# Kernel optimization log

Measured on AMD Instinct MI355X. Metric: run time of the kernel, lower is better.

The kernel has to match this reference:

```python
import jax, jax.numpy as jnp
import numpy as np

B, C_IN, T, H, W = 8, 8, 12, 128, 128
HID = 32
K = 3


def _conv2d(x, w, b):
    # x: (B, Cin, H, W), w: (Cout, Cin, K, K) -> SAME padding, stride 1
    y = jax.lax.conv_general_dilated(
        x, w, window_strides=(1, 1), padding='SAME',
        dimension_numbers=('NCHW', 'OIHW', 'NCHW'))
    return y + b[None, :, None, None]


def setup_inputs() -> dict:
    key = jax.random.key(0)
    k1, k2, k3, k4, k5 = jax.random.split(key, 5)
    x = jax.random.normal(k1, (B, C_IN, T, H, W), dtype=jnp.float32)
    cin = C_IN + HID
    scale = 1.0 / np.sqrt(cin * K * K)
    W_gates = jax.random.normal(k2, (2 * HID, cin, K, K), dtype=jnp.float32) * scale
    b_gates = jax.random.normal(k3, (2 * HID,), dtype=jnp.float32) * 0.01
    W_can = jax.random.normal(k4, (HID, cin, K, K), dtype=jnp.float32) * scale
    b_can = jax.random.normal(k5, (HID,), dtype=jnp.float32) * 0.01
    return {"x": x, "W_gates": W_gates, "b_gates": b_gates,
            "W_can": W_can, "b_can": b_can}


def reference(x, W_gates, b_gates, W_can, b_can):
    # x: (B, C, T, H, W) -> swap to time-major for the recurrence
    xs = jnp.transpose(x, (2, 0, 1, 3, 4))  # (T, B, C, H, W)
    h0 = jnp.zeros((x.shape[0], HID, x.shape[3], x.shape[4]), dtype=x.dtype)

    def step(h, x_t):
        comb = jnp.concatenate([x_t, h], axis=1)          # (B, C+HID, H, W)
        gates = jax.nn.sigmoid(_conv2d(comb, W_gates, b_gates))
        reset, update = jnp.split(gates, 2, axis=1)       # each (B, HID, H, W)
        comb2 = jnp.concatenate([x_t, reset * h], axis=1)
        cand = jnp.tanh(_conv2d(comb2, W_can, b_can))
        h_next = (1.0 - update) * h + update * cand
        return h_next, h_next

    h_last, ys = jax.lax.scan(step, h0, xs)               # ys: (T, B, HID, H, W)
    out = jnp.transpose(ys, (1, 2, 0, 3, 4))              # (B, HID, T, H, W) — swap back
    return out, h_last
```

## Files before the change

kernel.cpp:

```cpp
#include <hip/hip_runtime.h>
#include <hip/hip_bf16.h>
#include <hip/hip_fp16.h>
#include <cmath>

#define BB   8
#define CIN  8
#define TT   12
#define HH   128
#define WW   128
#define HID  32
#define CCOMB 40
#define HW   (HH * WW)
#define NBLK 512

#define S1    44
#define T1W   20
#define OFF2  17600
#define S2    36
#define OFFU  29264
#define SMEM_U16 38480

typedef __attribute__((ext_vector_type(8))) short sv8;
typedef __attribute__((ext_vector_type(4))) short sv4;
typedef __attribute__((ext_vector_type(4))) float f32x4;
typedef unsigned short u16;
typedef unsigned long long ull;

__device__ inline u16 f2bf(float f) {
    union { float f; unsigned u; } v; v.f = f;
    unsigned u = v.u;
    return (u16)((u + 0x7FFFu + ((u >> 16) & 1u)) >> 16);
}
__device__ inline float bf2f(u16 h) {
    union { unsigned u; float f; } v; v.u = ((unsigned)h) << 16; return v.f;
}
__device__ inline float sigmoid_fast(float x) { return 1.f / (1.f + __expf(-x)); }
__device__ inline float tanh_fast(float z) {
    float a = fabsf(z);
    float r = 1.f - 2.f / (__expf(2.f * a) + 1.f);
    return copysignf(r, z);
}

__device__ __forceinline__ void band_rc(int i, int& r, int& c) {
    if (i < 40)      { r = i / 20;            c = i % 20; }
    else if (i < 80) { int j = i - 40; r = 18 + j / 20; c = j % 20; }
    else             { int j = i - 80; r = 2 + (j >> 2);
                       int k = j & 3;  c = (k < 2) ? k : 16 + k; }
}

__device__ inline sv8 gather_wfrag(const float* __restrict__ W,
                                   int co, int g, int kx, int ks) {
    int k0 = ks * 32 + g * 8;
    sv8 f;
    if (k0 < 120) {
        int ky  = k0 / 40;
        int ci0 = k0 - ky * 40;
#pragma unroll
        for (int i = 0; i < 8; ++i)
            f[i] = (short)f2bf(W[(((size_t)co * CCOMB + ci0 + i) * 3 + ky) * 3 + kx]);
    } else {
#pragma unroll
        for (int i = 0; i < 8; ++i) f[i] = 0;
    }
    return f;
}

__global__ void pack_weights(const float* __restrict__ Wg,
                             const float* __restrict__ Wc,
                             u16* __restrict__ pack) {
    int tid = blockIdx.x * blockDim.x + threadIdx.x;
    if (tid >= 6 * 12 * 64) return;
    int lane = tid & 63;
    int f    = (tid >> 6) % 12;
    int Gall = tid / (12 * 64);
    int kx = f >> 2, ks = f & 3;
    int g = lane >> 4;
    sv8 v;
    if (Gall < 4) v = gather_wfrag(Wg, Gall * 16 + (lane & 15), g, kx, ks);
    else          v = gather_wfrag(Wc, (Gall - 4) * 16 + (lane & 15), g, kx, ks);
    *(sv8*)&pack[(size_t)tid * 8] = v;
}

__global__ __launch_bounds__(256) void x_to_bf16(const float* __restrict__ x,
                                                 u16* __restrict__ xbf) {
    int gid = blockIdx.x * 256 + threadIdx.x;
    if (gid >= BB * TT * HW) return;
    int p  = gid & (HW - 1);
    int bt = gid >> 14;
    int t = bt % TT, b = bt / TT;
    sv8 v;
#pragma unroll
    for (int c = 0; c < 8; ++c)
        v[c] = (short)f2bf(x[(((size_t)b * CIN + c) * TT + t) * HW + p]);
    *(sv8*)&xbf[(size_t)gid * 8] = v;
}

__global__ __launch_bounds__(256, 2) void gru_persist(
    const u16* __restrict__ xbf, const u16* __restrict__ wpack,
    const float* __restrict__ bg, const float* __restrict__ bc,
    u16* __restrict__ hG, int* __restrict__ flags,
    float* __restrict__ out, float* __restrict__ hlast)
{
    __shared__ __align__(16) u16 smem[SMEM_U16];
    const int id = blockIdx.x;
    const int b = id & 7, tau = id >> 3;
    const int bx = tau & 7, by = tau >> 3;
    const int x0 = bx * 16, y0 = by * 16;
    const int tid = threadIdx.x, lane = tid & 63, w = tid >> 6;
    const int m = lane & 15, g = lane >> 4;

    int nbr = -1;
    if (tid < 8) {
        const int dxs[8] = {-1, 0, 1, -1, 1, -1, 0, 1};
        const int dys[8] = {-1, -1, -1, 0, 0, 1, 1, 1};
        int nx = bx + dxs[tid], ny = by + dys[tid];
        if ((unsigned)nx < 8u && (unsigned)ny < 8u)
            nbr = ((ny * 8 + nx) * 8 + b);
    }

    int kyv[4], ci0v[4], koff1[4], coffC[4], kstrC[4];
    bool isX[4];
#pragma unroll
    for (int ks = 0; ks < 4; ++ks) {
        int k0 = ks * 32 + g * 8;
        int ky = 0, ci0 = 0;
        if (k0 < 120) { ky = k0 / 40; ci0 = k0 - ky * 40; }
        kyv[ks] = ky; ci0v[ks] = ci0;
        koff1[ks] = ky * (T1W * S1) + ci0;
        isX[ks]   = (ci0 == 0);
        coffC[ks] = isX[ks] ? ky * (T1W * S1) : ky * (18 * S2) + (ci0 - 8);
        kstrC[ks] = isX[ks] ? S1 : S2;
    }

    const int coPair = w >> 1;
    const int parity = w & 1;
    const int co0A = coPair * 32 + g * 4;
    const int co0B = co0A + 16;
    const int grpA = coPair * 2, grpB = grpA + 1;

    for (int i = tid; i < 3200; i += 256) {
        int px = i >> 3, q = i & 7;
        *(ull*)&smem[px * S1 + 8 + q * 4] = 0ull;
    }

    const u16* xbB = xbf + (size_t)b * TT * HW * 8;
    const size_t planeElems = (size_t)BB * HW * 32;

    for (int t = 0; t < TT; ++t) {
        const u16* hGr = hG + (size_t)(t & 1) * planeElems + (size_t)b * HW * 32;
        u16*       hGw = hG + (size_t)((t + 1) & 1) * planeElems + (size_t)b * HW * 32;

        sv8 wfA[12], wfB[12];
#pragma unroll
        for (int f = 0; f < 12; ++f) {
            wfA[f] = *(const sv8*)&wpack[(((size_t)grpA * 12 + f) * 64 + lane) * 8];
            wfB[f] = *(const sv8*)&wpack[(((size_t)grpB * 12 + f) * 64 + lane) * 8];
        }

        const u16* xb = xbB + (size_t)t * HW * 8;
        for (int idx = tid; idx < 400; idx += 256) {
            int r = idx / 20, c = idx - r * 20;
            int gy = y0 + r - 2, gx = x0 + c - 2;
            sv8 v = {};
            if ((unsigned)gy < 128u && (unsigned)gx < 128u)
                v = *(const sv8*)&xb[(size_t)(gy * WW + gx) * 8];
            *(sv4*)&smem[idx * S1]     = __builtin_shufflevector(v, v, 0,1,2,3);
            *(sv4*)&smem[idx * S1 + 4] = __builtin_shufflevector(v, v, 4,5,6,7);
        }

        if (t > 0) {
            if (tid < 8 && nbr >= 0) {
                while (__hip_atomic_load(&flags[nbr * 32], __ATOMIC_RELAXED,
                                         __HIP_MEMORY_SCOPE_AGENT) < t)
                    __builtin_amdgcn_s_sleep(8);
            }
            __syncthreads();
        }

        for (int idx = tid; idx < 1152; idx += 256) {
            int i = idx >> 3, q = idx & 7;
            int r, c; band_rc(i, r, c);
            int gy = y0 + r - 2, gx = x0 + c - 2;
            ull v = 0;
            if ((unsigned)gy < 128u && (unsigned)gx < 128u)
                v = __hip_atomic_load((const ull*)&hGr[(size_t)(gy * WW + gx) * 32 + q * 4],
                                      __ATOMIC_RELAXED, __HIP_MEMORY_SCOPE_AGENT);
            *(ull*)&smem[(r * T1W + c) * S1 + 8 + q * 4] = v;
        }
        __syncthreads();

        f32x4 bgA = *(const f32x4*)&bg[co0A];
        f32x4 bgB = *(const f32x4*)&bg[co0B];
        for (int nt = parity; nt < 21; nt += 2) {
            int px = nt * 16 + m;
            bool val = px < 324;
            if (!val) px = 323;
            int yy = px / 18, xx = px - yy * 18;
            int pb = (yy * T1W + xx) * S1;
            f32x4 aA = {0.f,0.f,0.f,0.f}, aB = {0.f,0.f,0.f,0.f};
#pragma unroll
            for (int kx = 0; kx < 3; ++kx)
#pragma unroll
                for (int ks = 0; ks < 4; ++ks) {
                    int a = pb + kx * S1 + koff1[ks];
                    sv4 lo = *(const sv4*)&smem[a];
                    sv4 hi = *(const sv4*)&smem[a + 4];
                    sv8 bv = __builtin_shufflevector(lo, hi, 0,1,2,3,4,5,6,7);
                    aA = __builtin_amdgcn_mfma_f32_16x16x32_bf16(wfA[kx*4+ks], bv, aA, 0, 0, 0);
                    aB = __builtin_amdgcn_mfma_f32_16x16x32_bf16(wfB[kx*4+ks], bv, aB, 0, 0, 0);
                }
            if (coPair == 0) {
                int ctr = pb + 21 * S1 + 8;
                sv4 h4A = *(const sv4*)&smem[ctr + co0A];
                sv4 h4B = *(const sv4*)&smem[ctr + co0B];
                sv4 rhA, rhB;
#pragma unroll
                for (int r = 0; r < 4; ++r) {
                    rhA[r] = (short)f2bf(sigmoid_fast(aA[r] + bgA[r]) * bf2f((u16)h4A[r]));
                    rhB[r] = (short)f2bf(sigmoid_fast(aB[r] + bgB[r]) * bf2f((u16)h4B[r]));
                }
                if (val) {
                    *(sv4*)&smem[OFF2 + px * S2 + co0A] = rhA;
                    *(sv4*)&smem[OFF2 + px * S2 + co0B] = rhB;
                }
            } else {
                sv4 uA, uB;
#pragma unroll
                for (int r = 0; r < 4; ++r) {
                    uA[r] = (short)__half_as_ushort(__float2half(sigmoid_fast(aA[r] + bgA[r])));
                    uB[r] = (short)__half_as_ushort(__float2half(sigmoid_fast(aB[r] + bgB[r])));
                }
                if (val && yy >= 1 && yy <= 16 && xx >= 1 && xx <= 16) {
                    int ub = OFFU + ((yy - 1) * 16 + (xx - 1)) * S2;
                    *(sv4*)&smem[ub + (co0A - 32)] = uA;
                    *(sv4*)&smem[ub + (co0B - 32)] = uB;
                }
            }
        }

        sv8 wcA[12], wcB[12];
#pragma unroll
        for (int f = 0; f < 12; ++f) {
            wcA[f] = *(const sv8*)&wpack[(((size_t)4 * 12 + f) * 64 + lane) * 8];
            wcB[f] = *(const sv8*)&wpack[(((size_t)5 * 12 + f) * 64 + lane) * 8];
        }
        __syncthreads();

        const int j0 = w * 4;
        int rowb1[4], rowb2[4];
#pragma unroll
        for (int jr = 0; jr < 4; ++jr) {
            rowb1[jr] = ((j0 + jr + 1) * T1W + m + 1) * S1;
            rowb2[jr] = OFF2 + ((j0 + jr) * 18 + m) * S2;
        }
        f32x4 a2A[4], a2B[4];
#pragma unroll
        for (int jr = 0; jr < 4; ++jr) {
            a2A[jr] = (f32x4){0.f,0.f,0.f,0.f};
            a2B[jr] = (f32x4){0.f,0.f,0.f,0.f};
        }
#pragma unroll
        for (int kx = 0; kx < 3; ++kx)
#pragma unroll
            for (int ks = 0; ks < 4; ++ks) {
#pragma unroll
                for (int jr = 0; jr < 4; ++jr) {
                    int a = (isX[ks] ? rowb1[jr] : rowb2[jr]) + coffC[ks] + kx * kstrC[ks];
                    sv4 lo = *(const sv4*)&smem[a];
                    sv4 hi = *(const sv4*)&smem[a + 4];
                    sv8 bv = __builtin_shufflevector(lo, hi, 0,1,2,3,4,5,6,7);
                    a2A[jr] = __builtin_amdgcn_mfma_f32_16x16x32_bf16(wcA[kx*4+ks], bv, a2A[jr], 0, 0, 0);
                    a2B[jr] = __builtin_amdgcn_mfma_f32_16x16x32_bf16(wcB[kx*4+ks], bv, a2B[jr], 0, 0, 0);
                }
            }

        f32x4 bcA = *(const f32x4*)&bc[g * 4];
        f32x4 bcB = *(const f32x4*)&bc[16 + g * 4];
        const int cA = g * 4, cB = 16 + g * 4;
#pragma unroll
        for (int jr = 0; jr < 4; ++jr) {
            int j = j0 + jr;
            int gy = y0 + j, gx = x0 + m;
            int ctr = ((j + 2) * T1W + m + 2) * S1 + 8;
            int ub  = OFFU + (j * 16 + m) * S2;
            sv4 h4A = *(const sv4*)&smem[ctr + cA];
            sv4 h4B = *(const sv4*)&smem[ctr + cB];
            sv4 u4A = *(const sv4*)&smem[ub + cA];
            sv4 u4B = *(const sv4*)&smem[ub + cB];
            sv4 hnA, hnB;
#pragma unroll
            for (int r = 0; r < 4; ++r) {
                float cv = tanh_fast(a2A[jr][r] + bcA[r]);
                float uu = __half2float(__ushort_as_half((u16)u4A[r]));
                float hn = (1.f - uu) * bf2f((u16)h4A[r]) + uu * cv;
                a2A[jr][r] = hn; hnA[r] = (short)f2bf(hn);
                cv = tanh_fast(a2B[jr][r] + bcB[r]);
                uu = __half2float(__ushort_as_half((u16)u4B[r]));
                hn = (1.f - uu) * bf2f((u16)h4B[r]) + uu * cv;
                a2B[jr][r] = hn; hnB[r] = (short)f2bf(hn);
            }
            *(sv4*)&smem[ctr + cA] = hnA;
            *(sv4*)&smem[ctr + cB] = hnB;
            if (j <= 1 || j >= 14 || m <= 1 || m >= 14) {
                union { sv4 s; ull u; } ca, cb; ca.s = hnA; cb.s = hnB;
                ull* base = (ull*)&hGw[(size_t)(gy * WW + gx) * 32];
                __hip_atomic_store(base + (cA >> 2), ca.u, __ATOMIC_RELAXED,
                                   __HIP_MEMORY_SCOPE_AGENT);
                __hip_atomic_store(base + (cB >> 2), cb.u, __ATOMIC_RELAXED,
                                   __HIP_MEMORY_SCOPE_AGENT);
            }
        }

        asm volatile("s_waitcnt vmcnt(0)" ::: "memory");
        __syncthreads();
        if (tid == 0)
            __hip_atomic_store(&flags[id * 32], t + 1, __ATOMIC_RELAXED,
                               __HIP_MEMORY_SCOPE_AGENT);

#pragma unroll
        for (int jr = 0; jr < 4; ++jr) {
            int j = j0 + jr;
            int gy = y0 + j, gx = x0 + m;
#pragma unroll
            for (int r = 0; r < 4; ++r) {
                __builtin_nontemporal_store(a2A[jr][r],
                    &out[(((size_t)b * HID + cA + r) * TT + t) * HW + (size_t)gy * WW + gx]);
                __builtin_nontemporal_store(a2B[jr][r],
                    &out[(((size_t)b * HID + cB + r) * TT + t) * HW + (size_t)gy * WW + gx]);
                if (t == TT - 1) {
                    __builtin_nontemporal_store(a2A[jr][r],
                        &hlast[((size_t)b * HID + cA + r) * HW + (size_t)gy * WW + gx]);
                    __builtin_nontemporal_store(a2B[jr][r],
                        &hlast[((size_t)b * HID + cB + r) * HW + (size_t)gy * WW + gx]);
                }
            }
        }
    }
}

extern "C" void kernel_launch(void* const* d_in, const int* in_sizes, int n_in,
                              void* d_out, int out_size, void* d_ws, size_t ws_size,
                              hipStream_t stream) {
    const float* x  = (const float*)d_in[0];
    const float* Wg = (const float*)d_in[1];
    const float* bg = (const float*)d_in[2];
    const float* Wc = (const float*)d_in[3];
    const float* bc = (const float*)d_in[4];

    float* out   = (float*)d_out;
    float* hlast = out + (size_t)BB * HID * TT * HW;

    const size_t PLANEB = (size_t)BB * HW * 32 * sizeof(u16);
    const size_t PACKB  = (size_t)6 * 12 * 64 * 8 * sizeof(u16);
    const size_t FLAGB  = (size_t)NBLK * 32 * sizeof(int);
    char* ws = (char*)d_ws;
    u16* hG    = (u16*)ws;
    u16* wpack = (u16*)(ws + 2 * PLANEB);
    int* flags = (int*)(ws + 2 * PLANEB + PACKB);
    u16* xbf   = (u16*)(ws + 2 * PLANEB + PACKB + FLAGB);

    pack_weights<<<(6 * 12 * 64 + 255) / 256, 256, 0, stream>>>(Wg, Wc, wpack);
    x_to_bf16<<<(BB * TT * HW) / 256, 256, 0, stream>>>(x, xbf);
    hipMemsetAsync(hG, 0, PLANEB, stream);
    hipMemsetAsync(flags, 0, FLAGB, stream);

    gru_persist<<<NBLK, 256, 0, stream>>>(xbf, wpack, bg, bc, hG, flags,
                                          out, hlast);
}
```

Baseline: 464.2 us.

## Compute interior gate tiles before waiting on neighbor halo flags

The gates convolution is split into interior pixels, whose stencil needs only the block's own previous h, and halo-ring pixels. Interior tiles are now computed before the spin-wait on neighbor flags, so that work overlaps the cross-block synchronization. The ring tiles run after the neighbor halo is loaded. Index math and bias loads are hoisted out of the time loop and the sleep interval is shortened, at the cost of an extra barrier per step and more registers.

Result: slower. 554.6 us (+19.5%).

```diff
diff --git a/kernel.cpp b/kernel.cpp
--- a/kernel.cpp
+++ b/kernel.cpp
@@ -95,6 +95,50 @@
     *(sv8*)&xbf[(size_t)gid * 8] = v;
 }
 
+#define MFMA16(A, B, C) __builtin_amdgcn_mfma_f32_16x16x32_bf16(A, B, C, 0, 0, 0)
+
+#define GATES_TILE(PB, OFF2V, UOFFV, LVAL, UVALQ)                              \
+    {                                                                          \
+        f32x4 aA = {0.f,0.f,0.f,0.f}, aB = {0.f,0.f,0.f,0.f};                  \
+        _Pragma("unroll")                                                      \
+        for (int kx = 0; kx < 3; ++kx)                                         \
+        _Pragma("unroll")                                                      \
+        for (int ks = 0; ks < 4; ++ks) {                                       \
+            int a = (PB) + kx * S1 + koff1[ks];                                \
+            sv4 lo = *(const sv4*)&smem[a];                                    \
+            sv4 hi = *(const sv4*)&smem[a + 4];                                \
+            sv8 bv = __builtin_shufflevector(lo, hi, 0,1,2,3,4,5,6,7);         \
+            aA = MFMA16(wfA[kx*4+ks], bv, aA);                                 \
+            aB = MFMA16(wfB[kx*4+ks], bv, aB);                                 \
+        }                                                                      \
+        if (coPair == 0) {                                                     \
+            int ctr = (PB) + 21 * S1 + 8;                                      \
+            sv4 h4A = *(const sv4*)&smem[ctr + co0A];                          \
+            sv4 h4B = *(const sv4*)&smem[ctr + co0B];                          \
+            sv4 rhA, rhB;                                                      \
+            _Pragma("unroll")                                                  \
+            for (int r = 0; r < 4; ++r) {                                      \
+                rhA[r] = (short)f2bf(sigmoid_fast(aA[r] + bgA[r]) * bf2f((u16)h4A[r])); \
+                rhB[r] = (short)f2bf(sigmoid_fast(aB[r] + bgB[r]) * bf2f((u16)h4B[r])); \
+            }                                                                  \
+            if (LVAL) {                                                        \
+                *(sv4*)&smem[(OFF2V) + co0A] = rhA;                            \
+                *(sv4*)&smem[(OFF2V) + co0B] = rhB;                            \
+            }                                                                  \
+        } else {                                                               \
+            sv4 uA, uB;                                                        \
+            _Pragma("unroll")                                                  \
+            for (int r = 0; r < 4; ++r) {                                      \
+                uA[r] = (short)__half_as_ushort(__float2half(sigmoid_fast(aA[r] + bgA[r]))); \
+                uB[r] = (short)__half_as_ushort(__float2half(sigmoid_fast(aB[r] + bgB[r]))); \
+            }                                                                  \
+            if ((LVAL) && (UVALQ)) {                                           \
+                *(sv4*)&smem[(UOFFV) + (co0A - 32)] = uA;                      \
+                *(sv4*)&smem[(UOFFV) + (co0B - 32)] = uB;                      \
+            }                                                                  \
+        }                                                                      \
+    }
+
 __global__ __launch_bounds__(256, 2) void gru_persist(
     const u16* __restrict__ xbf, const u16* __restrict__ wpack,
     const float* __restrict__ bg, const float* __restrict__ bc,
@@ -118,14 +162,13 @@
             nbr = ((ny * 8 + nx) * 8 + b);
     }
 
-    int kyv[4], ci0v[4], koff1[4], coffC[4], kstrC[4];
+    int koff1[4], coffC[4], kstrC[4];
     bool isX[4];
 #pragma unroll
     for (int ks = 0; ks < 4; ++ks) {
         int k0 = ks * 32 + g * 8;
         int ky = 0, ci0 = 0;
         if (k0 < 120) { ky = k0 / 40; ci0 = k0 - ky * 40; }
-        kyv[ks] = ky; ci0v[ks] = ci0;
         koff1[ks] = ky * (T1W * S1) + ci0;
         isX[ks]   = (ci0 == 0);
         coffC[ks] = isX[ks] ? ky * (T1W * S1) : ky * (18 * S2) + (ci0 - 8);
@@ -137,6 +180,49 @@
     const int co0A = coPair * 32 + g * 4;
     const int co0B = co0A + 16;
     const int grpA = coPair * 2, grpB = grpA + 1;
+
+    int ipb[7], i2[7], iu[7]; bool ivalid[7], ilane[7];
+#pragma unroll
+    for (int k = 0; k < 7; ++k) {
+        int nt = parity + 2 * k;
+        ivalid[k] = (nt < 13);
+        int i = nt * 16 + m;
+        ilane[k] = ivalid[k] && (i < 196);
+        if (i > 195) i = 195;
+        int yy = 2 + i / 14, xx = 2 + (i % 14);
+        ipb[k] = (yy * T1W + xx) * S1;
+        i2[k]  = OFF2 + (yy * 18 + xx) * S2;
+        iu[k]  = OFFU + ((yy - 1) * 16 + (xx - 1)) * S2;
+    }
+    int epb[4], e2[4], eu[4]; bool euval[4];
+#pragma unroll
+    for (int k = 0; k < 4; ++k) {
+        int nt = parity + 2 * k;
+        int e = nt * 16 + m;
+        int yy, xx;
+        if (e < 36)       { yy = e / 18;               xx = e - (e / 18) * 18; }
+        else if (e < 72)  { int j = e - 36; yy = 16 + j / 18; xx = j - (j / 18) * 18; }
+        else if (e < 100) { int j = e - 72;  yy = 2 + (j >> 1); xx = (j & 1); }
+        else              { int j = e - 100; yy = 2 + (j >> 1); xx = 16 + (j & 1); }
+        epb[k] = (yy * T1W + xx) * S1;
+        e2[k]  = OFF2 + (yy * 18 + xx) * S2;
+        euval[k] = (yy >= 1 && yy <= 16 && xx >= 1 && xx <= 16);
+        eu[k]  = OFFU + ((yy - 1) * 16 + (xx - 1)) * S2;
+    }
+
+    const int j0 = w * 4;
+    int rowb1[4], rowb2[4];
+#pragma unroll
+    for (int jr = 0; jr < 4; ++jr) {
+        rowb1[jr] = ((j0 + jr + 1) * T1W + m + 1) * S1;
+        rowb2[jr] = OFF2 + ((j0 + jr) * 18 + m) * S2;
+    }
+
+    f32x4 bgA = *(const f32x4*)&bg[co0A];
+    f32x4 bgB = *(const f32x4*)&bg[co0B];
+    f32x4 bcA = *(const f32x4*)&bc[g * 4];
+    f32x4 bcB = *(const f32x4*)&bc[16 + g * 4];
+    const int cA = g * 4, cB = 16 + g * 4;
 
     for (int i = tid; i < 3200; i += 256) {
         int px = i >> 3, q = i & 7;
@@ -167,15 +253,21 @@
             *(sv4*)&smem[idx * S1]     = __builtin_shufflevector(v, v, 0,1,2,3);
             *(sv4*)&smem[idx * S1 + 4] = __builtin_shufflevector(v, v, 4,5,6,7);
         }
+        __syncthreads();
+
+#pragma unroll
+        for (int k = 0; k < 7; ++k)
+            if (ivalid[k])
+                GATES_TILE(ipb[k], i2[k], iu[k], ilane[k], true);
 
         if (t > 0) {
             if (tid < 8 && nbr >= 0) {
                 while (__hip_atomic_load(&flags[nbr * 32], __ATOMIC_RELAXED,
                                          __HIP_MEMORY_SCOPE_AGENT) < t)
-                    __builtin_amdgcn_s_sleep(8);
+                    __builtin_amdgcn_s_sleep(4);
             }
-            __syncthreads();
-        }
+        }
+        __syncthreads();
 
         for (int idx = tid; idx < 1152; idx += 256) {
             int i = idx >> 3, q = idx & 7;
@@ -187,56 +279,6 @@
                                       __ATOMIC_RELAXED, __HIP_MEMORY_SCOPE_AGENT);
             *(ull*)&smem[(r * T1W + c) * S1 + 8 + q * 4] = v;
         }
-        __syncthreads();
-
-        f32x4 bgA = *(const f32x4*)&bg[co0A];
-        f32x4 bgB = *(const f32x4*)&bg[co0B];
-        for (int nt = parity; nt < 21; nt += 2) {
-            int px = nt * 16 + m;
-            bool val = px < 324;
-            if (!val) px = 323;
-            int yy = px / 18, xx = px - yy * 18;
-            int pb = (yy * T1W + xx) * S1;
-            f32x4 aA = {0.f,0.f,0.f,0.f}, aB = {0.f,0.f,0.f,0.f};
-#pragma unroll
-            for (int kx = 0; kx < 3; ++kx)
-#pragma unroll
-                for (int ks = 0; ks < 4; ++ks) {
-                    int a = pb + kx * S1 + koff1[ks];
-                    sv4 lo = *(const sv4*)&smem[a];
-                    sv4 hi = *(const sv4*)&smem[a + 4];
-                    sv8 bv = __builtin_shufflevector(lo, hi, 0,1,2,3,4,5,6,7);
-                    aA = __builtin_amdgcn_mfma_f32_16x16x32_bf16(wfA[kx*4+ks], bv, aA, 0, 0, 0);
-                    aB = __builtin_amdgcn_mfma_f32_16x16x32_bf16(wfB[kx*4+ks], bv, aB, 0, 0, 0);
-                }
-            if (coPair == 0) {
-                int ctr = pb + 21 * S1 + 8;
-                sv4 h4A = *(const sv4*)&smem[ctr + co0A];
-                sv4 h4B = *(const sv4*)&smem[ctr + co0B];
-                sv4 rhA, rhB;
-#pragma unroll
-                for (int r = 0; r < 4; ++r) {
-                    rhA[r] = (short)f2bf(sigmoid_fast(aA[r] + bgA[r]) * bf2f((u16)h4A[r]));
-                    rhB[r] = (short)f2bf(sigmoid_fast(aB[r] + bgB[r]) * bf2f((u16)h4B[r]));
-                }
-                if (val) {
-                    *(sv4*)&smem[OFF2 + px * S2 + co0A] = rhA;
-                    *(sv4*)&smem[OFF2 + px * S2 + co0B] = rhB;
-                }
-            } else {
-                sv4 uA, uB;
-#pragma unroll
-                for (int r = 0; r < 4; ++r) {
-                    uA[r] = (short)__half_as_ushort(__float2half(sigmoid_fast(aA[r] + bgA[r])));
-                    uB[r] = (short)__half_as_ushort(__float2half(sigmoid_fast(aB[r] + bgB[r])));
-                }
-                if (val && yy >= 1 && yy <= 16 && xx >= 1 && xx <= 16) {
-                    int ub = OFFU + ((yy - 1) * 16 + (xx - 1)) * S2;
-                    *(sv4*)&smem[ub + (co0A - 32)] = uA;
-                    *(sv4*)&smem[ub + (co0B - 32)] = uB;
-                }
-            }
-        }
 
         sv8 wcA[12], wcB[12];
 #pragma unroll
@@ -246,13 +288,11 @@
         }
         __syncthreads();
 
-        const int j0 = w * 4;
-        int rowb1[4], rowb2[4];
-#pragma unroll
-        for (int jr = 0; jr < 4; ++jr) {
-            rowb1[jr] = ((j0 + jr + 1) * T1W + m + 1) * S1;
-            rowb2[jr] = OFF2 + ((j0 + jr) * 18 + m) * S2;
-        }
+#pragma unroll
+        for (int k = 0; k < 4; ++k)
+            GATES_TILE(epb[k], e2[k], eu[k], true, euval[k]);
+        __syncthreads();
+
         f32x4 a2A[4], a2B[4];
 #pragma unroll
         for (int jr = 0; jr < 4; ++jr) {
@@ -269,14 +309,11 @@
                     sv4 lo = *(const sv4*)&smem[a];
                     sv4 hi = *(const sv4*)&smem[a + 4];
                     sv8 bv = __builtin_shufflevector(lo, hi, 0,1,2,3,4,5,6,7);
-                    a2A[jr] = __builtin_amdgcn_mfma_f32_16x16x32_bf16(wcA[kx*4+ks], bv, a2A[jr], 0, 0, 0);
-                    a2B[jr] = __builtin_amdgcn_mfma_f32_16x16x32_bf16(wcB[kx*4+ks], bv, a2B[jr], 0, 0, 0);
+                    a2A[jr] = MFMA16(wcA[kx*4+ks], bv, a2A[jr]);
+                    a2B[jr] = MFMA16(wcB[kx*4+ks], bv, a2B[jr]);
                 }
             }
 
-        f32x4 bcA = *(const f32x4*)&bc[g * 4];
-        f32x4 bcB = *(const f32x4*)&bc[16 + g * 4];
-        const int cA = g * 4, cB = 16 + g * 4;
 #pragma unroll
         for (int jr = 0; jr < 4; ++jr) {
             int j = j0 + jr;
```
